# Optimization experiments

Hardware: AMD Instinct MI355X
Metric: run time of the kernel (lower is better)

## Reference

```python
import jax, jax.numpy as jnp
import numpy as np

B, N, C = 4, 4096, 256  # batch, num_points, channels (in=out=key)
LN_EPS = 1e-6
STAB = 1e-9


def setup_inputs() -> dict:
    key = jax.random.key(0)
    ks = jax.random.split(key, 12)
    s = 0.02
    return {
        "inputs": jax.random.normal(ks[0], (B, N, C), jnp.float32),
        "mask": jax.random.randint(ks[1], (B, N), 0, 2).astype(bool),
        "Wq": s * jax.random.normal(ks[2], (C, C), jnp.float32),
        "bq": jnp.zeros((C,), jnp.float32),
        "Wk": s * jax.random.normal(ks[3], (C, C), jnp.float32),
        "bk": jnp.zeros((C,), jnp.float32),
        "Wv": s * jax.random.normal(ks[4], (C, C), jnp.float32),
        "bv": jnp.zeros((C,), jnp.float32),
        "Wo": s * jax.random.normal(ks[5], (C, C), jnp.float32),
        "bo": jnp.zeros((C,), jnp.float32),
        "ln_scale": jnp.ones((C,), jnp.float32),
        "ln_bias": jnp.zeros((C,), jnp.float32),
    }


def reference(inputs, mask, Wq, bq, Wk, bk, Wv, bv, Wo, bo, ln_scale, ln_bias):
    # kernel_size=1 Conv == pointwise dense
    q = inputs @ Wq + bq  # [B,N,C]
    k = inputs @ Wk + bk
    v = inputs @ Wv + bv
    att = jnp.einsum('bmc,bnc->bmn', q, k)  # [B,M,N]
    attn_mask = mask[:, :, None] & mask[:, None, :]  # make_attention_mask then squeeze
    big_neg = jnp.finfo(att.dtype).min
    att = jnp.where(attn_mask, att, big_neg)
    att = jax.nn.softmax(att, axis=-1)
    # extra renormalization over the M (query) axis
    att = att / (STAB + jnp.sum(att, axis=1, keepdims=True))
    # NOTE: faithful to source einsum '...MN,...NC->...NC' (sums over M only)
    out = jnp.einsum('bmn,bnc->bnc', att, v)  # [B,N,C]
    out = out @ Wo + bo
    # LayerNorm with reduction_axes=-2 (normalize over points axis)
    mean = jnp.mean(out, axis=-2, keepdims=True)
    var = jnp.mean(jnp.square(out), axis=-2, keepdims=True) - jnp.square(mean)
    out = (out - mean) * jax.lax.rsqrt(var + LN_EPS) * ln_scale + ln_bias
    out = jax.nn.relu(out)
    return out + inputs
```

## Files before the change

kernel.cpp:

```cpp
#include <hip/hip_runtime.h>
#include <math.h>

#define BATCH 4
#define NPTS 4096
#define CH 256
#define LN_EPS 1e-6f

typedef __attribute__((ext_vector_type(8))) _Float16 half8;
typedef __attribute__((ext_vector_type(4))) float f32x4;

__global__ __launch_bounds__(256) void fuse_weights(
    const float* __restrict__ Wv, const float* __restrict__ bv,
    const float* __restrict__ Wo, const float* __restrict__ bo,
    _Float16* __restrict__ Wct, float* __restrict__ bc,
    float* __restrict__ accg) {
    const int j = threadIdx.x;
    const int i = blockIdx.x;
    if (i < CH) {
        float acc = 0.f;
        #pragma unroll 4
        for (int c = 0; c < CH; c += 4) {
            const float4 wv = *(const float4*)&Wv[i * CH + c];
            acc = fmaf(wv.x, Wo[(c + 0) * CH + j], acc);
            acc = fmaf(wv.y, Wo[(c + 1) * CH + j], acc);
            acc = fmaf(wv.z, Wo[(c + 2) * CH + j], acc);
            acc = fmaf(wv.w, Wo[(c + 3) * CH + j], acc);
        }
        Wct[(size_t)j * CH + i] = (_Float16)acc;
    } else {
        float acc = bo[j];
        #pragma unroll 4
        for (int c = 0; c < CH; c += 4) {
            const float4 bv4 = *(const float4*)&bv[c];
            acc = fmaf(bv4.x, Wo[(c + 0) * CH + j], acc);
            acc = fmaf(bv4.y, Wo[(c + 1) * CH + j], acc);
            acc = fmaf(bv4.z, Wo[(c + 2) * CH + j], acc);
            acc = fmaf(bv4.w, Wo[(c + 3) * CH + j], acc);
        }
        bc[j] = acc;
        #pragma unroll
        for (int t = 0; t < 2 * BATCH; ++t)
            accg[t * CH + j] = 0.f;
    }
}

#define APAD 40
#define BPAD 264
#define BST_BYTES (64 * BPAD * 2)
#define POOL_BYTES (BST_BYTES + 64 * APAD * 2)
#define TPAD 68

__global__ __launch_bounds__(256) void gemm_fused(
    const float* __restrict__ A, const _Float16* __restrict__ Wct,
    const float* __restrict__ bc, float* __restrict__ u,
    float* __restrict__ accg) {
    __shared__ __align__(16) char pool[POOL_BYTES];
    _Float16* Bst = (_Float16*)pool;
    _Float16* As  = (_Float16*)(pool + BST_BYTES);
    float*    Tr  = (float*)pool;

    const int tid = threadIdx.x;
    const int m0 = blockIdx.x * 64;
    const int n0 = blockIdx.y * 64;
    const int w = tid >> 6;
    const int l = tid & 63;
    const int lr = l & 15;
    const int lq = l >> 4;

    {
        const int nr = tid >> 2;
        const int ks = (tid & 3) * 64;
        #pragma unroll
        for (int i = 0; i < 8; ++i)
            *(half8*)&Bst[nr * BPAD + ks + i * 8] =
                *(const half8*)&Wct[(size_t)(n0 + nr) * CH + ks + i * 8];
    }

    f32x4 acc[4];
    #pragma unroll
    for (int f = 0; f < 4; ++f) acc[f] = (f32x4){0.f, 0.f, 0.f, 0.f};

    const int arow = tid >> 2;
    const int akseg = (tid & 3) * 8;

    for (int kc = 0; kc < CH; kc += 32) {
        const float* aptr = &A[(size_t)(m0 + arow) * CH + kc + akseg];
        const float4 a0 = *(const float4*)aptr;
        const float4 a1 = *(const float4*)(aptr + 4);
        half8 ah;
        ah[0] = (_Float16)a0.x; ah[1] = (_Float16)a0.y;
        ah[2] = (_Float16)a0.z; ah[3] = (_Float16)a0.w;
        ah[4] = (_Float16)a1.x; ah[5] = (_Float16)a1.y;
        ah[6] = (_Float16)a1.z; ah[7] = (_Float16)a1.w;

        __syncthreads();
        *(half8*)&As[arow * APAD + akseg] = ah;
        __syncthreads();

        const half8 afrag = *(const half8*)&As[(w * 16 + lr) * APAD + lq * 8];
        #pragma unroll
        for (int f = 0; f < 4; ++f) {
            const half8 bfrag =
                *(const half8*)&Bst[(f * 16 + lr) * BPAD + kc + lq * 8];
            acc[f] = __builtin_amdgcn_mfma_f32_16x16x32_f16(afrag, bfrag, acc[f], 0, 0, 0);
        }
    }

    const int batch = m0 >> 12;
    #pragma unroll
    for (int f = 0; f < 4; ++f) {
        const int n = n0 + f * 16 + lr;
        const float bcn = bc[n];
        float s1 = 0.f, s2 = 0.f;
        #pragma unroll
        for (int r = 0; r < 4; ++r) {
            const float v = acc[f][r] + bcn;
            acc[f][r] = v;
            s1 += v;
            s2 = fmaf(v, v, s2);
        }
        s1 += __shfl_xor(s1, 16, 64);
        s1 += __shfl_xor(s1, 32, 64);
        s2 += __shfl_xor(s2, 16, 64);
        s2 += __shfl_xor(s2, 32, 64);
        if (lq == 0) {
            atomicAdd(&accg[batch * CH + n], s1);
            atomicAdd(&accg[BATCH * CH + batch * CH + n], s2);
        }
    }

    __syncthreads();
    #pragma unroll
    for (int f = 0; f < 4; ++f)
        #pragma unroll
        for (int r = 0; r < 4; ++r)
            Tr[(w * 16 + lq * 4 + r) * TPAD + f * 16 + lr] = acc[f][r];
    __syncthreads();

    {
        const int row = tid >> 4;
        const int grp = tid & 15;
        #pragma unroll
        for (int j = 0; j < 4; ++j) {
            const int rr = row + j * 16;
            const float4 v = *(const float4*)&Tr[rr * TPAD + grp * 4];
            *(float4*)&u[(size_t)(m0 + rr) * CH + n0 + grp * 4] = v;
        }
    }
}

__global__ __launch_bounds__(256) void ln_finish(
    const float* __restrict__ u, const float* __restrict__ inp,
    const float* __restrict__ accg, const float* __restrict__ scale,
    const float* __restrict__ bias, float* __restrict__ out) {
    const int idx = blockIdx.x * blockDim.x + threadIdx.x;
    const int c4 = (idx & 63) * 4;
    const int bn = idx >> 6;
    const int b = bn >> 12;
    const size_t off = (size_t)idx * 4;

    const float4 uv = *(const float4*)&u[off];
    const float4 xv = *(const float4*)&inp[off];
    const float4 s1 = *(const float4*)&accg[b * CH + c4];
    const float4 s2 = *(const float4*)&accg[BATCH * CH + b * CH + c4];
    const float4 sc = *(const float4*)&scale[c4];
    const float4 bi = *(const float4*)&bias[c4];

    const float invN = 1.f / (float)NPTS;
    float uu[4] = {uv.x, uv.y, uv.z, uv.w};
    float xx[4] = {xv.x, xv.y, xv.z, xv.w};
    float a1[4] = {s1.x, s1.y, s1.z, s1.w};
    float a2[4] = {s2.x, s2.y, s2.z, s2.w};
    float scv[4] = {sc.x, sc.y, sc.z, sc.w};
    float biv[4] = {bi.x, bi.y, bi.z, bi.w};
    float r[4];
    #pragma unroll
    for (int j = 0; j < 4; ++j) {
        const float mean = a1[j] * invN;
        const float var = a2[j] * invN - mean * mean;
        const float inv = rsqrtf(var + LN_EPS);
        float y = (uu[j] - mean) * inv * scv[j] + biv[j];
        r[j] = fmaxf(y, 0.f) + xx[j];
    }
    float4 ro;
    ro.x = r[0]; ro.y = r[1]; ro.z = r[2]; ro.w = r[3];
    *(float4*)&out[off] = ro;
}

extern "C" void kernel_launch(void* const* d_in, const int* in_sizes, int n_in,
                              void* d_out, int out_size, void* d_ws, size_t ws_size,
                              hipStream_t stream) {
    const float* inputs   = (const float*)d_in[0];
    const float* Wv       = (const float*)d_in[6];
    const float* bv       = (const float*)d_in[7];
    const float* Wo       = (const float*)d_in[8];
    const float* bo       = (const float*)d_in[9];
    const float* ln_scale = (const float*)d_in[10];
    const float* ln_bias  = (const float*)d_in[11];
    float* out = (float*)d_out;

    float*     u    = (float*)d_ws;
    float*     accg = (float*)((char*)d_ws + (size_t)BATCH * NPTS * CH * 4);
    _Float16*  Wct  = (_Float16*)((char*)accg + 2 * BATCH * CH * 4);
    float*     bc   = (float*)((char*)Wct + (size_t)CH * CH * 2);

    fuse_weights<<<CH + 1, 256, 0, stream>>>(Wv, bv, Wo, bo, Wct, bc, accg);
    gemm_fused<<<dim3((BATCH * NPTS) / 64, CH / 64), 256, 0, stream>>>(
        inputs, Wct, bc, u, accg);
    ln_finish<<<(BATCH * NPTS * CH / 4) / 256, 256, 0, stream>>>(
        u, inputs, accg, ln_scale, ln_bias, out);
}
```

Measured before the change: 119.5 us.

## Store intermediate in fp16, widen GEMM N-tile, batch weight-fusion rows

The intermediate pre-LayerNorm tensor is now stored as fp16 instead of fp32, which halves its write and read traffic between the GEMM and the LayerNorm finish kernel. The GEMM N tile grows from 64 to 128 so each A tile is loaded once per two column halves, and launch bounds now request occupancy of 2. The weight-fusion kernel computes 8 rows per block with one vectorized fp16 store, cutting the block count from 257 to 33. ln_finish processes 8 elements per thread. The cost is fp16 rounding of the intermediate before normalization and more register pressure in the GEMM.

```diff
diff --git a/kernel.cpp b/kernel.cpp
--- a/kernel.cpp
+++ b/kernel.cpp
@@ -15,18 +15,28 @@
     _Float16* __restrict__ Wct, float* __restrict__ bc,
     float* __restrict__ accg) {
     const int j = threadIdx.x;
-    const int i = blockIdx.x;
-    if (i < CH) {
-        float acc = 0.f;
-        #pragma unroll 4
+    const int blk = blockIdx.x;
+    if (blk < 32) {
+        const int i0 = blk * 8;
+        float acc[8] = {0.f, 0.f, 0.f, 0.f, 0.f, 0.f, 0.f, 0.f};
         for (int c = 0; c < CH; c += 4) {
-            const float4 wv = *(const float4*)&Wv[i * CH + c];
-            acc = fmaf(wv.x, Wo[(c + 0) * CH + j], acc);
-            acc = fmaf(wv.y, Wo[(c + 1) * CH + j], acc);
-            acc = fmaf(wv.z, Wo[(c + 2) * CH + j], acc);
-            acc = fmaf(wv.w, Wo[(c + 3) * CH + j], acc);
-        }
-        Wct[(size_t)j * CH + i] = (_Float16)acc;
+            const float wo0 = Wo[(c + 0) * CH + j];
+            const float wo1 = Wo[(c + 1) * CH + j];
+            const float wo2 = Wo[(c + 2) * CH + j];
+            const float wo3 = Wo[(c + 3) * CH + j];
+            #pragma unroll
+            for (int r = 0; r < 8; ++r) {
+                const float4 wv = *(const float4*)&Wv[(size_t)(i0 + r) * CH + c];
+                acc[r] = fmaf(wv.x, wo0, acc[r]);
+                acc[r] = fmaf(wv.y, wo1, acc[r]);
+                acc[r] = fmaf(wv.z, wo2, acc[r]);
+                acc[r] = fmaf(wv.w, wo3, acc[r]);
+            }
+        }
+        half8 hv;
+        #pragma unroll
+        for (int r = 0; r < 8; ++r) hv[r] = (_Float16)acc[r];
+        *(half8*)&Wct[(size_t)j * CH + i0] = hv;
     } else {
         float acc = bo[j];
         #pragma unroll 4
@@ -44,41 +54,43 @@
     }
 }
 
+#define TM 64
+#define TN 128
 #define APAD 40
 #define BPAD 264
-#define BST_BYTES (64 * BPAD * 2)
-#define POOL_BYTES (BST_BYTES + 64 * APAD * 2)
-#define TPAD 68
-
-__global__ __launch_bounds__(256) void gemm_fused(
+#define BST_BYTES (TN * BPAD * 2)
+#define POOL_BYTES (BST_BYTES + TM * APAD * 2)
+#define TPAD16 144
+
+__global__ __launch_bounds__(256, 2) void gemm_fused(
     const float* __restrict__ A, const _Float16* __restrict__ Wct,
-    const float* __restrict__ bc, float* __restrict__ u,
+    const float* __restrict__ bc, _Float16* __restrict__ u,
     float* __restrict__ accg) {
     __shared__ __align__(16) char pool[POOL_BYTES];
     _Float16* Bst = (_Float16*)pool;
     _Float16* As  = (_Float16*)(pool + BST_BYTES);
-    float*    Tr  = (float*)pool;
+    _Float16* Tr  = (_Float16*)pool;
 
     const int tid = threadIdx.x;
-    const int m0 = blockIdx.x * 64;
-    const int n0 = blockIdx.y * 64;
+    const int m0 = blockIdx.x * TM;
+    const int n0 = blockIdx.y * TN;
     const int w = tid >> 6;
     const int l = tid & 63;
     const int lr = l & 15;
     const int lq = l >> 4;
 
     {
-        const int nr = tid >> 2;
-        const int ks = (tid & 3) * 64;
-        #pragma unroll
-        for (int i = 0; i < 8; ++i)
+        const int nr = tid >> 1;
+        const int ks = (tid & 1) * 128;
+        #pragma unroll
+        for (int i = 0; i < 16; ++i)
             *(half8*)&Bst[nr * BPAD + ks + i * 8] =
                 *(const half8*)&Wct[(size_t)(n0 + nr) * CH + ks + i * 8];
     }
 
-    f32x4 acc[4];
-    #pragma unroll
-    for (int f = 0; f < 4; ++f) acc[f] = (f32x4){0.f, 0.f, 0.f, 0.f};
+    f32x4 acc[8];
+    #pragma unroll
+    for (int f = 0; f < 8; ++f) acc[f] = (f32x4){0.f, 0.f, 0.f, 0.f};
 
     const int arow = tid >> 2;
     const int akseg = (tid & 3) * 8;
@@ -99,7 +111,7 @@
 
         const half8 afrag = *(const half8*)&As[(w * 16 + lr) * APAD + lq * 8];
         #pragma unroll
-        for (int f = 0; f < 4; ++f) {
+        for (int f = 0; f < 8; ++f) {
             const half8 bfrag =
                 *(const half8*)&Bst[(f * 16 + lr) * BPAD + kc + lq * 8];
             acc[f] = __builtin_amdgcn_mfma_f32_16x16x32_f16(afrag, bfrag, acc[f], 0, 0, 0);
@@ -108,7 +120,7 @@
 
     const int batch = m0 >> 12;
     #pragma unroll
-    for (int f = 0; f < 4; ++f) {
+    for (int f = 0; f < 8; ++f) {
         const int n = n0 + f * 16 + lr;
         const float bcn = bc[n];
         float s1 = 0.f, s2 = 0.f;
@@ -131,10 +143,10 @@
 
     __syncthreads();
     #pragma unroll
-    for (int f = 0; f < 4; ++f)
+    for (int f = 0; f < 8; ++f)
         #pragma unroll
         for (int r = 0; r < 4; ++r)
-            Tr[(w * 16 + lq * 4 + r) * TPAD + f * 16 + lr] = acc[f][r];
+            Tr[(w * 16 + lq * 4 + r) * TPAD16 + f * 16 + lr] = (_Float16)acc[f][r];
     __syncthreads();
 
     {
@@ -143,48 +155,53 @@
         #pragma unroll
         for (int j = 0; j < 4; ++j) {
             const int rr = row + j * 16;
-            const float4 v = *(const float4*)&Tr[rr * TPAD + grp * 4];
-            *(float4*)&u[(size_t)(m0 + rr) * CH + n0 + grp * 4] = v;
+            const half8 v = *(const half8*)&Tr[rr * TPAD16 + grp * 8];
+            *(half8*)&u[(size_t)(m0 + rr) * CH + n0 + grp * 8] = v;
         }
     }
 }
 
 __global__ __launch_bounds__(256) void ln_finish(
-    const float* __restrict__ u, const float* __restrict__ inp,
+    const _Float16* __restrict__ u, const float* __restrict__ inp,
     const float* __restrict__ accg, const float* __restrict__ scale,
     const float* __restrict__ bias, float* __restrict__ out) {
     const int idx = blockIdx.x * blockDim.x + threadIdx.x;
-    const int c4 = (idx & 63) * 4;
-    const int bn = idx >> 6;
-    const int b = bn >> 12;
-    const size_t off = (size_t)idx * 4;
-
-    const float4 uv = *(const float4*)&u[off];
-    const float4 xv = *(const float4*)&inp[off];
-    const float4 s1 = *(const float4*)&accg[b * CH + c4];
-    const float4 s2 = *(const float4*)&accg[BATCH * CH + b * CH + c4];
-    const float4 sc = *(const float4*)&scale[c4];
-    const float4 bi = *(const float4*)&bias[c4];
+    const int c8 = (idx & 31) * 8;
+    const int b = idx >> 17;
+    const size_t off = (size_t)idx * 8;
+
+    const half8 uh = *(const half8*)&u[off];
+    const float4 x0 = *(const float4*)&inp[off];
+    const float4 x1 = *(const float4*)&inp[off + 4];
+    const float4 s1a = *(const float4*)&accg[b * CH + c8];
+    const float4 s1b = *(const float4*)&accg[b * CH + c8 + 4];
+    const float4 s2a = *(const float4*)&accg[BATCH * CH + b * CH + c8];
+    const float4 s2b = *(const float4*)&accg[BATCH * CH + b * CH + c8 + 4];
+    const float4 sca = *(const float4*)&scale[c8];
+    const float4 scb = *(const float4*)&scale[c8 + 4];
+    const float4 bia = *(const float4*)&bias[c8];
+    const float4 bib = *(const float4*)&bias[c8 + 4];
 
     const float invN = 1.f / (float)NPTS;
-    float uu[4] = {uv.x, uv.y, uv.z, uv.w};
-    float xx[4] = {xv.x, xv.y, xv.z, xv.w};
-    float a1[4] = {s1.x, s1.y, s1.z, s1.w};
-    float a2[4] = {s2.x, s2.y, s2.z, s2.w};
-    float scv[4] = {sc.x, sc.y, sc.z, sc.w};
-    float biv[4] = {bi.x, bi.y, bi.z, bi.w};
-    float r[4];
-    #pragma unroll
-    for (int j = 0; j < 4; ++j) {
+    float xx[8] = {x0.x, x0.y, x0.z, x0.w, x1.x, x1.y, x1.z, x1.w};
+    float a1[8] = {s1a.x, s1a.y, s1a.z, s1a.w, s1b.x, s1b.y, s1b.z, s1b.w};
+    float a2[8] = {s2a.x, s2a.y, s2a.z, s2a.w, s2b.x, s2b.y, s2b.z, s2b.w};
+    float scv[8] = {sca.x, sca.y, sca.z, sca.w, scb.x, scb.y, scb.z, scb.w};
+    float biv[8] = {bia.x, bia.y, bia.z, bia.w, bib.x, bib.y, bib.z, bib.w};
+    float r[8];
+    #pragma unroll
+    for (int j = 0; j < 8; ++j) {
         const float mean = a1[j] * invN;
         const float var = a2[j] * invN - mean * mean;
         const float inv = rsqrtf(var + LN_EPS);
-        float y = (uu[j] - mean) * inv * scv[j] + biv[j];
+        const float y = ((float)uh[j] - mean) * inv * scv[j] + biv[j];
         r[j] = fmaxf(y, 0.f) + xx[j];
     }
-    float4 ro;
-    ro.x = r[0]; ro.y = r[1]; ro.z = r[2]; ro.w = r[3];
-    *(float4*)&out[off] = ro;
+    float4 o0, o1;
+    o0.x = r[0]; o0.y = r[1]; o0.z = r[2]; o0.w = r[3];
+    o1.x = r[4]; o1.y = r[5]; o1.z = r[6]; o1.w = r[7];
+    *(float4*)&out[off] = o0;
+    *(float4*)&out[off + 4] = o1;
 }
 
 extern "C" void kernel_launch(void* const* d_in, const int* in_sizes, int n_in,
@@ -199,14 +216,14 @@
     const float* ln_bias  = (const float*)d_in[11];
     float* out = (float*)d_out;
 
-    float*     u    = (float*)d_ws;
-    float*     accg = (float*)((char*)d_ws + (size_t)BATCH * NPTS * CH * 4);
-    _Float16*  Wct  = (_Float16*)((char*)accg + 2 * BATCH * CH * 4);
-    float*     bc   = (float*)((char*)Wct + (size_t)CH * CH * 2);
-
-    fuse_weights<<<CH + 1, 256, 0, stream>>>(Wv, bv, Wo, bo, Wct, bc, accg);
-    gemm_fused<<<dim3((BATCH * NPTS) / 64, CH / 64), 256, 0, stream>>>(
+    _Float16* u    = (_Float16*)d_ws;
+    float*    accg = (float*)((char*)d_ws + (size_t)BATCH * NPTS * CH * 2);
+    _Float16* Wct  = (_Float16*)((char*)accg + 2 * BATCH * CH * 4);
+    float*    bc   = (float*)((char*)Wct + (size_t)CH * CH * 2);
+
+    fuse_weights<<<33, 256, 0, stream>>>(Wv, bv, Wo, bo, Wct, bc, accg);
+    gemm_fused<<<dim3((BATCH * NPTS) / TM, CH / TN), 256, 0, stream>>>(
         inputs, Wct, bc, u, accg);
-    ln_finish<<<(BATCH * NPTS * CH / 4) / 256, 256, 0, stream>>>(
+    ln_finish<<<(BATCH * NPTS * CH / 8) / 256, 256, 0, stream>>>(
         u, inputs, accg, ln_scale, ln_bias, out);
 }
```

Result: slower. 140.5 us (+17.6%).
